# Kernel optimization log

Measured on AMD Instinct MI355X. Metric: run time of the kernel, lower is better.

The kernel has to match this reference:

```python
import jax, jax.numpy as jnp
import numpy as np

N = 50000
E = 800000
IN_C = 128
HID = 128
NUM_CLASSES = 64


def setup_inputs() -> dict:
    key = jax.random.key(0)
    ks = jax.random.split(key, 8)
    x = jax.random.normal(ks[0], (N, IN_C), dtype=jnp.float32)
    edge_index = jax.random.randint(ks[1], (2, E), 0, N, dtype=jnp.int64)
    # Xavier-uniform style weights stored as [in, out]; biases zero-init.
    def xavier(k, fan_in, fan_out):
        lim = float(np.sqrt(6.0 / (fan_in + fan_out)))
        return jax.random.uniform(k, (fan_in, fan_out), minval=-lim, maxval=lim, dtype=jnp.float32)
    W1 = xavier(ks[2], IN_C, HID)
    b1 = jnp.zeros((HID,), dtype=jnp.float32)
    W2 = xavier(ks[3], HID, HID)
    b2 = jnp.zeros((HID,), dtype=jnp.float32)
    W3 = xavier(ks[4], HID, NUM_CLASSES)
    b3 = jnp.zeros((NUM_CLASSES,), dtype=jnp.float32)
    return {"x": x, "edge_index": edge_index, "W1": W1, "b1": b1, "W2": W2, "b2": b2, "W3": W3, "b3": b3}


def _add_self_loops(edge_index, num_nodes):
    loops = jnp.arange(num_nodes, dtype=edge_index.dtype)
    row = jnp.concatenate([edge_index[0], loops])
    col = jnp.concatenate([edge_index[1], loops])
    return row, col


def _gcn_layer(x, row, col, dinv, W, b):
    # x: [N, Cin] -> h: [N, Cout]; symmetric-normalized scatter-add aggregation.
    h = x @ W
    norm = dinv[row] * dinv[col]              # [E']
    msg = norm[:, None] * h[row]              # gather + scale (dropout is a no-op in eval)
    out = jax.ops.segment_sum(msg, col, num_segments=x.shape[0])
    return out + b


def reference(x, edge_index, W1, b1, W2, b2, W3, b3):
    n = x.shape[0]
    row, col = _add_self_loops(edge_index, n)
    deg = jax.ops.segment_sum(jnp.ones_like(col, dtype=x.dtype), col, num_segments=n)
    dinv = jnp.where(deg > 0, deg ** -0.5, 0.0)
    h1 = jax.nn.relu(_gcn_layer(x, row, col, dinv, W1, b1))
    h2 = jax.nn.relu(_gcn_layer(h1, row, col, dinv, W2, b2))
    out = _gcn_layer(h2, row, col, dinv, W3, b3)
    return (h2, out)
```

## Files before the change

### kernel.cpp

```cpp
#include <hip/hip_runtime.h>
#include <hip/hip_bf16.h>


typedef float vf4 __attribute__((ext_vector_type(4)));
typedef unsigned vu4 __attribute__((ext_vector_type(4)));
typedef unsigned vu2 __attribute__((ext_vector_type(2)));
typedef short bf8v __attribute__((ext_vector_type(8)));
typedef float f4v __attribute__((ext_vector_type(4)));

constexpr int PCAP = 25000;
constexpr int NHB  = 64;

__device__ __forceinline__ float bits2f(unsigned u) {
    union { unsigned u; float f; } c; c.u = u; return c.f;
}
__device__ __forceinline__ unsigned short f2bfu(float v) {
    __hip_bfloat16 h = __float2bfloat16(v);
    union { __hip_bfloat16 h; unsigned short u; } c; c.h = h; return c.u;
}
__device__ __forceinline__ float bflo(unsigned d) { return bits2f(d << 16); }
__device__ __forceinline__ float bfhi(unsigned d) { return bits2f(d & 0xffff0000u); }

__global__ void detect_dtypes(const void* __restrict__ x,
                              const void* __restrict__ ei,
                              int* __restrict__ flags) {
    const int t = threadIdx.x;
    const int lane = t & 63;
    if (t < 64) {
        const unsigned short* p = (const unsigned short*)x;
        int e = (p[2 * (lane * 16)] >> 7) & 0xFF;
        unsigned long long m = __ballot(e < 100 || e > 140);
        if (lane == 0) flags[0] = (__popcll(m) > 16) ? 1 : 0;
    } else if (t < 128) {
        const int* p = (const int*)ei;
        unsigned long long m = __ballot(p[2 * (lane * 16) + 1] != 0);
        if (lane == 0) flags[1] = (__popcll(m) < 2) ? 1 : 0;
    }
}

__device__ __forceinline__ int edge_at(const void* ei, long long idx, bool i64) {
    return i64 ? (int)((const long long*)ei)[idx] : ((const int*)ei)[idx];
}

__global__ __launch_bounds__(1024) void hist_count(const void* __restrict__ ei,
                                                   int* __restrict__ row32,
                                                   int* __restrict__ col32,
                                                   unsigned* __restrict__ histg,
                                                   const int* __restrict__ flags,
                                                   int e, int epb, int pc) {
    __shared__ unsigned h[PCAP];
    const int t = threadIdx.x;
    const int b = blockIdx.x;
    for (int j = t; j < pc; j += 1024) h[j] = 0u;
    __syncthreads();
    const bool i64 = flags[1] != 0;
    const int base = b * epb;
    const int end = min(e, base + epb);
    for (int i = base + t; i < end; i += 1024) {
        int r = edge_at(ei, i, i64);
        int c = edge_at(ei, (long long)e + i, i64);
        row32[i] = r;
        col32[i] = c;
        atomicAdd(&h[c >> 1], (c & 1) ? 0x10000u : 1u);
    }
    __syncthreads();
    unsigned* out = histg + (size_t)b * pc;
    for (int j = t; j < pc; j += 1024) __builtin_nontemporal_store(h[j], &out[j]);
}

__global__ __launch_bounds__(256) void hist_scan(unsigned* __restrict__ histg,
                                                 int* __restrict__ cnt, int pc, int n) {
    __shared__ unsigned tile[NHB][65];
    const int t = threadIdx.x;
    const int c = t & 63;
    const int jc = blockIdx.x * 64 + c;
    for (int r = t >> 6; r < NHB; r += 4)
        tile[r][c] = (jc < pc) ? histg[(size_t)r * pc + jc] : 0u;
    __syncthreads();
    if (t < 64 && jc < pc) {
        unsigned run = 0;
        for (int r = 0; r < NHB; ++r) {
            unsigned v = tile[r][t];
            tile[r][t] = run;
            run += v;
        }
        int c0 = jc * 2;
        if (c0 < n) cnt[c0] = (int)(run & 0xffffu);
        if (c0 + 1 < n) cnt[c0 + 1] = (int)(run >> 16);
    }
    __syncthreads();
    for (int r = t >> 6; r < NHB; r += 4)
        if (jc < pc) __builtin_nontemporal_store(tile[r][c], &histg[(size_t)r * pc + jc]);
}

__global__ __launch_bounds__(1024) void scatter_fill(const int* __restrict__ row32,
                                                     const int* __restrict__ col32,
                                                     const unsigned* __restrict__ histg,
                                                     const int* __restrict__ off,
                                                     int* __restrict__ csr,
                                                     int e, int epb, int pc) {
    __shared__ unsigned h[PCAP];
    const int t = threadIdx.x;
    const int b = blockIdx.x;
    const unsigned* src = histg + (size_t)b * pc;
    for (int j = t; j < pc; j += 1024) h[j] = src[j];
    __syncthreads();
    const int base = b * epb;
    const int end = min(e, base + epb);
    for (int i = base + t; i < end; i += 1024) {
        int r = row32[i];
        int c = col32[i];
        unsigned old = atomicAdd(&h[c >> 1], (c & 1) ? 0x10000u : 1u);
        unsigned rank = (c & 1) ? (old >> 16) : (old & 0xffffu);
        csr[off[c] + (int)rank] = r;
    }
}

__global__ void convert_count(const void* __restrict__ ei,
                              int* __restrict__ row32, int* __restrict__ col32,
                              int* __restrict__ rank32,
                              int* __restrict__ cnt,
                              const int* __restrict__ flags, int e) {
    int i = blockIdx.x * 256 + threadIdx.x;
    if (i < e) {
        const bool i64 = flags[1] != 0;
        int r = edge_at(ei, i, i64);
        int c = edge_at(ei, (long long)e + i, i64);
        row32[i] = r;
        col32[i] = c;
        rank32[i] = atomicAdd(&cnt[c], 1);
    }
}

__global__ void fill_csr(const int* __restrict__ row32, const int* __restrict__ col32,
                         const int* __restrict__ rank32, const int* __restrict__ off,
                         int* __restrict__ csr_src, int e) {
    int i = blockIdx.x * 256 + threadIdx.x;
    if (i < e) {
        csr_src[off[col32[i]] + rank32[i]] = row32[i];
    }
}

__global__ __launch_bounds__(256) void deg_reduce(const int* __restrict__ cnt,
                                                  int* __restrict__ bsum, int n) {
    __shared__ int sm[4];
    const int t = threadIdx.x;
    int i = blockIdx.x * 256 + t;
    int v = (i < n) ? cnt[i] : 0;
#pragma unroll
    for (int d = 32; d >= 1; d >>= 1) v += __shfl_down(v, d);
    if ((t & 63) == 0) sm[t >> 6] = v;
    __syncthreads();
    if (t == 0) bsum[blockIdx.x] = sm[0] + sm[1] + sm[2] + sm[3];
}

__global__ __launch_bounds__(256) void scan_bsums(int* __restrict__ bsum, int nb) {
    __shared__ int sm[256];
    const int t = threadIdx.x;
    sm[t] = (t < nb) ? bsum[t] : 0;
    __syncthreads();
#pragma unroll
    for (int d = 1; d < 256; d <<= 1) {
        int v = (t >= d) ? sm[t - d] : 0;
        __syncthreads();
        sm[t] += v;
        __syncthreads();
    }
    if (t < nb) bsum[t] = (t == 0) ? 0 : sm[t - 1];
}

__global__ __launch_bounds__(256) void write_off(const int* __restrict__ cnt,
                                                 const int* __restrict__ bsum,
                                                 int* __restrict__ off,
                                                 float* __restrict__ dinv,
                                                 int n, int e_total) {
    __shared__ int sm[256];
    const int t = threadIdx.x;
    const int i = blockIdx.x * 256 + t;
    const int c = (i < n) ? cnt[i] : 0;
    sm[t] = c;
    __syncthreads();
#pragma unroll
    for (int d = 1; d < 256; d <<= 1) {
        int v = (t >= d) ? sm[t - d] : 0;
        __syncthreads();
        sm[t] += v;
        __syncthreads();
    }
    if (i < n) {
        int o = bsum[blockIdx.x] + sm[t] - c;
        off[i] = o;
        dinv[i] = rsqrtf((float)(c + 1));
        if (i == n - 1) off[n] = e_total;
    }
}

template <int COUT, bool XDYN>
__global__ __launch_bounds__(256) void gemm_mfma(const void* __restrict__ Xv,
                                                 const void* __restrict__ Wv,
                                                 const float* __restrict__ dinv,
                                                 unsigned short* __restrict__ G,
                                                 const int* __restrict__ flags, int n) {
    constexpr int WS = 132;
    __shared__ __align__(16) short Wt[COUT * WS];
    const int t = threadIdx.x;
    const bool f32 = flags[0] != 0;

    if (f32) {
        const float* W = (const float*)Wv;
        for (int i = t; i < 128 * COUT; i += 256) {
            int k = i / COUT, c = i % COUT;
            Wt[c * WS + k] = (short)f2bfu(W[i]);
        }
    } else {
        const short* W = (const short*)Wv;
        for (int i = t; i < 128 * COUT; i += 256) {
            int k = i / COUT, c = i % COUT;
            Wt[c * WS + k] = W[i];
        }
    }
    __syncthreads();

    const int w = t >> 6, l = t & 63;
    const int m = l & 15, q = l >> 4;
    const int row = blockIdx.x * 64 + w * 16 + m;
    const int xrow = min(row, n - 1);

    bf8v xf[4];
    if (XDYN && f32) {
        const float* X = (const float*)Xv;
#pragma unroll
        for (int ks = 0; ks < 4; ++ks) {
            const float4 a = *(const float4*)&X[(size_t)xrow * 128 + ks * 32 + q * 8];
            const float4 b = *(const float4*)&X[(size_t)xrow * 128 + ks * 32 + q * 8 + 4];
            bf8v v;
            v[0] = (short)f2bfu(a.x); v[1] = (short)f2bfu(a.y);
            v[2] = (short)f2bfu(a.z); v[3] = (short)f2bfu(a.w);
            v[4] = (short)f2bfu(b.x); v[5] = (short)f2bfu(b.y);
            v[6] = (short)f2bfu(b.z); v[7] = (short)f2bfu(b.w);
            xf[ks] = v;
        }
    } else {
        const short* X = (const short*)Xv;
#pragma unroll
        for (int ks = 0; ks < 4; ++ks)
            xf[ks] = *(const bf8v*)&X[(size_t)xrow * 128 + ks * 32 + q * 8];
    }
    const float dv = dinv[xrow];

#pragma unroll
    for (int ct = 0; ct < COUT / 16; ++ct) {
        f4v acc = {0.f, 0.f, 0.f, 0.f};
#pragma unroll
        for (int ks = 0; ks < 4; ++ks) {
            bf8v wf = *(const bf8v*)&Wt[(ct * 16 + m) * WS + ks * 32 + q * 8];
            acc = __builtin_amdgcn_mfma_f32_16x16x32_bf16(wf, xf[ks], acc, 0, 0, 0);
        }
        if (row < n) {
            vu2 u;
            u.x = (unsigned)f2bfu(dv * acc[0]) | ((unsigned)f2bfu(dv * acc[1]) << 16);
            u.y = (unsigned)f2bfu(dv * acc[2]) | ((unsigned)f2bfu(dv * acc[3]) << 16);
            *(vu2*)&G[(size_t)row * COUT + ct * 16 + q * 4] = u;
        }
    }
}

template <int CPL, bool RELU, bool WWS, bool WOUT>
__global__ __launch_bounds__(256) void aggregate(const unsigned* __restrict__ Gd,
                                                 const int* __restrict__ off,
                                                 const int* __restrict__ csr_src,
                                                 const float* __restrict__ dinv,
                                                 const void* __restrict__ bias,
                                                 unsigned* __restrict__ Hws,
                                                 void* __restrict__ outp,
                                                 long long out_off,
                                                 const int* __restrict__ flags, int n) {
    const int gw = (int)((blockIdx.x * 256u + threadIdx.x) >> 6);
    const int lane = threadIdx.x & 63;
    if (gw >= n) return;
    constexpr int C = CPL * 64;
    constexpr int LPG = (CPL == 2) ? 16 : 8;
    constexpr int GROUPS = 64 / LPG;
    constexpr int RD = C / 2;
    const int g = lane / LPG;
    const int li = lane % LPG;
    const int e0 = off[gw];
    const int e1 = off[gw + 1];
    const float d = dinv[gw];

    float acc[8];
    {
        uint4 sv = *(const uint4*)&Gd[(size_t)gw * RD + li * 4];
        const float ms = (g == 0) ? 1.f : 0.f;
        acc[0] = ms * bflo(sv.x); acc[1] = ms * bfhi(sv.x);
        acc[2] = ms * bflo(sv.y); acc[3] = ms * bfhi(sv.y);
        acc[4] = ms * bflo(sv.z); acc[5] = ms * bfhi(sv.z);
        acc[6] = ms * bflo(sv.w); acc[7] = ms * bfhi(sv.w);
    }

    for (int bs = e0; bs < e1; bs += 64) {
        const int cnt = min(64, e1 - bs);
        const int myidx = (bs + lane < e1) ? csr_src[bs + lane] : 0;
        for (int j = 0; j < cnt; j += 2 * GROUPS) {
#pragma unroll
            for (int u = 0; u < 2; ++u) {
                const int eb = j + u * GROUPS + g;
                const int jj = min(eb, cnt - 1);
                const int s = __shfl(myidx, jj);
                const float m = (eb < cnt) ? 1.f : 0.f;
                uint4 v = *(const uint4*)&Gd[(size_t)s * RD + li * 4];
                acc[0] = fmaf(m, bflo(v.x), acc[0]);
                acc[1] = fmaf(m, bfhi(v.x), acc[1]);
                acc[2] = fmaf(m, bflo(v.y), acc[2]);
                acc[3] = fmaf(m, bfhi(v.y), acc[3]);
                acc[4] = fmaf(m, bflo(v.z), acc[4]);
                acc[5] = fmaf(m, bfhi(v.z), acc[5]);
                acc[6] = fmaf(m, bflo(v.w), acc[6]);
                acc[7] = fmaf(m, bfhi(v.w), acc[7]);
            }
        }
    }

#pragma unroll
    for (int mask = LPG; mask <= 32; mask <<= 1)
#pragma unroll
        for (int i = 0; i < 8; ++i) acc[i] += __shfl_xor(acc[i], mask);

    const bool f32 = flags[0] != 0;
    float bvf[8];
    if (f32) {
        const float* B = (const float*)bias;
        const float4 b0 = *(const float4*)&B[li * 8];
        const float4 b1 = *(const float4*)&B[li * 8 + 4];
        bvf[0] = b0.x; bvf[1] = b0.y; bvf[2] = b0.z; bvf[3] = b0.w;
        bvf[4] = b1.x; bvf[5] = b1.y; bvf[6] = b1.z; bvf[7] = b1.w;
    } else {
        const uint4 bv = *(const uint4*)&((const unsigned*)bias)[li * 4];
        bvf[0] = bflo(bv.x); bvf[1] = bfhi(bv.x);
        bvf[2] = bflo(bv.y); bvf[3] = bfhi(bv.y);
        bvf[4] = bflo(bv.z); bvf[5] = bfhi(bv.z);
        bvf[6] = bflo(bv.w); bvf[7] = bfhi(bv.w);
    }
    float o[8];
#pragma unroll
    for (int i = 0; i < 8; ++i) {
        o[i] = d * acc[i] + bvf[i];
        if (RELU) o[i] = fmaxf(o[i], 0.f);
    }

    if (g == 0) {
        if constexpr (WWS) {
            vu4 u;
            u.x = (unsigned)f2bfu(o[0]) | ((unsigned)f2bfu(o[1]) << 16);
            u.y = (unsigned)f2bfu(o[2]) | ((unsigned)f2bfu(o[3]) << 16);
            u.z = (unsigned)f2bfu(o[4]) | ((unsigned)f2bfu(o[5]) << 16);
            u.w = (unsigned)f2bfu(o[6]) | ((unsigned)f2bfu(o[7]) << 16);
            unsigned* hb = Hws + (size_t)gw * RD + li * 4;
            __builtin_nontemporal_store(u, (vu4*)hb);
        }
        if constexpr (WOUT) {
            if (f32) {
                float* po = (float*)outp + out_off + (size_t)gw * C + li * 8;
                vf4 w0 = {o[0], o[1], o[2], o[3]};
                vf4 w1 = {o[4], o[5], o[6], o[7]};
                __builtin_nontemporal_store(w0, (vf4*)po);
                __builtin_nontemporal_store(w1, (vf4*)po + 1);
            } else {
                vu4 u;
                u.x = (unsigned)f2bfu(o[0]) | ((unsigned)f2bfu(o[1]) << 16);
                u.y = (unsigned)f2bfu(o[2]) | ((unsigned)f2bfu(o[3]) << 16);
                u.z = (unsigned)f2bfu(o[4]) | ((unsigned)f2bfu(o[5]) << 16);
                u.w = (unsigned)f2bfu(o[6]) | ((unsigned)f2bfu(o[7]) << 16);
                unsigned* ob = (unsigned*)outp + (out_off >> 1) + (size_t)gw * RD + li * 4;
                __builtin_nontemporal_store(u, (vu4*)ob);
            }
        }
    }
}

extern "C" void kernel_launch(void* const* d_in, const int* in_sizes, int n_in,
                              void* d_out, int out_size, void* d_ws, size_t ws_size,
                              hipStream_t stream) {
    const void* x  = d_in[0];
    const void* ei = d_in[1];
    const void* W1 = d_in[2];
    const void* b1 = d_in[3];
    const void* W2 = d_in[4];
    const void* b2 = d_in[5];
    const void* W3 = d_in[6];
    const void* b3 = d_in[7];

    const int N = in_sizes[0] / 128;
    const int E = in_sizes[1] / 2;

    char* p = (char*)d_ws;
    auto take = [&](size_t bytes) {
        char* q = p;
        p += (bytes + 255) & ~(size_t)255;
        return q;
    };
    const int pc  = (N + 1) / 2;
    const int epb = (E + NHB - 1) / NHB;
    const bool histpath = (pc <= PCAP) && (epb < 65536);

    int*      flags = (int*)take(64);
    int*      cnt   = (int*)take((size_t)N * 4);
    int*      bsum  = (int*)take(1024);
    int*      off   = (int*)take((size_t)(N + 1) * 4);
    float*    dinv  = (float*)take((size_t)N * 4);
    int*      row32 = (int*)take((size_t)E * 4);
    int*      col32 = (int*)take((size_t)E * 4);
    int*      csr   = (int*)take((size_t)E * 4);
    unsigned* histg = (unsigned*)take(histpath ? (size_t)NHB * pc * 4 : 0);
    int*      rank32 = (int*)take(histpath ? 0 : (size_t)E * 4);
    unsigned short* bufA = (unsigned short*)take((size_t)N * 128 * 2);
    unsigned short* bufB = (unsigned short*)take((size_t)N * 128 * 2);
    (void)n_in; (void)out_size; (void)ws_size;

    const int nb = (N + 255) / 256;
    const int eb = (E + 255) / 256;

    detect_dtypes<<<1, 128, 0, stream>>>(x, ei, flags);

    if (histpath) {
        hist_count<<<NHB, 1024, 0, stream>>>(ei, row32, col32, histg, flags, E, epb, pc);
        hist_scan<<<(pc + 63) / 64, 256, 0, stream>>>(histg, cnt, pc, N);
        deg_reduce<<<nb, 256, 0, stream>>>(cnt, bsum, N);
        scan_bsums<<<1, 256, 0, stream>>>(bsum, nb);
        write_off<<<nb, 256, 0, stream>>>(cnt, bsum, off, dinv, N, E);
        scatter_fill<<<NHB, 1024, 0, stream>>>(row32, col32, histg, off, csr, E, epb, pc);
    } else {
        hipMemsetAsync(cnt, 0, (size_t)N * 4, stream);
        convert_count<<<eb, 256, 0, stream>>>(ei, row32, col32, rank32, cnt, flags, E);
        deg_reduce<<<nb, 256, 0, stream>>>(cnt, bsum, N);
        scan_bsums<<<1, 256, 0, stream>>>(bsum, nb);
        write_off<<<nb, 256, 0, stream>>>(cnt, bsum, off, dinv, N, E);
        fill_csr<<<eb, 256, 0, stream>>>(row32, col32, rank32, off, csr, E);
    }

    const int gb = (N + 63) / 64;
    const int ab = (N + 3) / 4;

    gemm_mfma<128, true><<<gb, 256, 0, stream>>>(x, W1, dinv, bufA, flags, N);
    aggregate<2, true, true, false><<<ab, 256, 0, stream>>>((const unsigned*)bufA, off, csr, dinv, b1, (unsigned*)bufB, nullptr, 0, flags, N);
    gemm_mfma<128, false><<<gb, 256, 0, stream>>>(bufB, W2, dinv, bufA, flags, N);
    aggregate<2, true, true, true><<<ab, 256, 0, stream>>>((const unsigned*)bufA, off, csr, dinv, b2, (unsigned*)bufB, d_out, 0, flags, N);
    gemm_mfma<64, false><<<gb, 256, 0, stream>>>(bufB, W3, dinv, bufA, flags, N);
    aggregate<1, false, false, true><<<ab, 256, 0, stream>>>((const unsigned*)bufA, off, csr, dinv, b3, nullptr, d_out, (long long)N * 128, flags, N);
}
```

Baseline: 277.1 us.

## Fuse degree reduce into hist scan, drop row32/col32 staging, double hist blocks

The CSR build no longer stages int32 row/col copies. hist_count reads only the column array, and scatter_fill re-reads the original edge_index directly. hist_scan now processes 128 packed columns (256 nodes) per block and emits per-block degree sums, which removes the separate deg_reduce launch. The number of histogram blocks doubles to 128 for more parallelism, at the cost of a larger histogram buffer and a longer serial scan per column. Re-reading the int64 edge indices in scatter_fill may cost more bandwidth than reading the int32 copies did.

```diff
diff --git a/kernel.cpp b/kernel.cpp
--- a/kernel.cpp
+++ b/kernel.cpp
@@ -9,7 +9,8 @@
 typedef float f4v __attribute__((ext_vector_type(4)));
 
 constexpr int PCAP = 25000;
-constexpr int NHB  = 64;
+constexpr int NHB  = 128;
+constexpr int SCB  = 128;
 
 __device__ __forceinline__ float bits2f(unsigned u) {
     union { unsigned u; float f; } c; c.u = u; return c.f;
@@ -43,8 +44,6 @@
 }
 
 __global__ __launch_bounds__(1024) void hist_count(const void* __restrict__ ei,
-                                                   int* __restrict__ row32,
-                                                   int* __restrict__ col32,
                                                    unsigned* __restrict__ histg,
                                                    const int* __restrict__ flags,
                                                    int e, int epb, int pc) {
@@ -52,6 +51,72 @@
     const int t = threadIdx.x;
     const int b = blockIdx.x;
     for (int j = t; j < pc; j += 1024) h[j] = 0u;
+    __syncthreads();
+    const bool i64 = flags[1] != 0;
+    const int base = b * epb;
+    const int end = min(e, base + epb);
+    for (int i = base + t; i < end; i += 1024) {
+        int c = edge_at(ei, (long long)e + i, i64);
+        atomicAdd(&h[c >> 1], (c & 1) ? 0x10000u : 1u);
+    }
+    __syncthreads();
+    unsigned* out = histg + (size_t)b * pc;
+    for (int j = t; j < pc; j += 1024) __builtin_nontemporal_store(h[j], &out[j]);
+}
+
+__global__ __launch_bounds__(256) void hist_scan(unsigned* __restrict__ histg,
+                                                 int* __restrict__ cnt,
+                                                 int* __restrict__ bsum,
+                                                 int pc, int n) {
+    __shared__ unsigned tile[NHB][SCB + 1];
+    __shared__ int red[2];
+    const int t = threadIdx.x;
+    const int b = blockIdx.x;
+    const int jc0 = b * SCB;
+    for (int idx = t; idx < NHB * SCB; idx += 256) {
+        int r = idx >> 7;
+        int c = idx & (SCB - 1);
+        int jc = jc0 + c;
+        tile[r][c] = (jc < pc) ? histg[(size_t)r * pc + jc] : 0u;
+    }
+    __syncthreads();
+    int deg = 0;
+    if (t < SCB) {
+        unsigned run = 0;
+        for (int r = 0; r < NHB; ++r) {
+            unsigned v = tile[r][t];
+            tile[r][t] = run;
+            run += v;
+        }
+        int c0 = (jc0 + t) * 2;
+        if (c0 < n) cnt[c0] = (int)(run & 0xffffu);
+        if (c0 + 1 < n) cnt[c0 + 1] = (int)(run >> 16);
+        deg = (int)(run & 0xffffu) + (int)(run >> 16);
+    }
+#pragma unroll
+    for (int d2 = 32; d2 >= 1; d2 >>= 1) deg += __shfl_down(deg, d2);
+    if ((t & 63) == 0 && t < SCB) red[t >> 6] = deg;
+    __syncthreads();
+    if (t == 0) bsum[b] = red[0] + red[1];
+    for (int idx = t; idx < NHB * SCB; idx += 256) {
+        int r = idx >> 7;
+        int c = idx & (SCB - 1);
+        int jc = jc0 + c;
+        if (jc < pc) __builtin_nontemporal_store(tile[r][c], &histg[(size_t)r * pc + jc]);
+    }
+}
+
+__global__ __launch_bounds__(1024) void scatter_fill(const void* __restrict__ ei,
+                                                     const unsigned* __restrict__ histg,
+                                                     const int* __restrict__ off,
+                                                     int* __restrict__ csr,
+                                                     const int* __restrict__ flags,
+                                                     int e, int epb, int pc) {
+    __shared__ unsigned h[PCAP];
+    const int t = threadIdx.x;
+    const int b = blockIdx.x;
+    const unsigned* src = histg + (size_t)b * pc;
+    for (int j = t; j < pc; j += 1024) h[j] = src[j];
     __syncthreads();
     const bool i64 = flags[1] != 0;
     const int base = b * epb;
@@ -59,57 +124,6 @@
     for (int i = base + t; i < end; i += 1024) {
         int r = edge_at(ei, i, i64);
         int c = edge_at(ei, (long long)e + i, i64);
-        row32[i] = r;
-        col32[i] = c;
-        atomicAdd(&h[c >> 1], (c & 1) ? 0x10000u : 1u);
-    }
-    __syncthreads();
-    unsigned* out = histg + (size_t)b * pc;
-    for (int j = t; j < pc; j += 1024) __builtin_nontemporal_store(h[j], &out[j]);
-}
-
-__global__ __launch_bounds__(256) void hist_scan(unsigned* __restrict__ histg,
-                                                 int* __restrict__ cnt, int pc, int n) {
-    __shared__ unsigned tile[NHB][65];
-    const int t = threadIdx.x;
-    const int c = t & 63;
-    const int jc = blockIdx.x * 64 + c;
-    for (int r = t >> 6; r < NHB; r += 4)
-        tile[r][c] = (jc < pc) ? histg[(size_t)r * pc + jc] : 0u;
-    __syncthreads();
-    if (t < 64 && jc < pc) {
-        unsigned run = 0;
-        for (int r = 0; r < NHB; ++r) {
-            unsigned v = tile[r][t];
-            tile[r][t] = run;
-            run += v;
-        }
-        int c0 = jc * 2;
-        if (c0 < n) cnt[c0] = (int)(run & 0xffffu);
-        if (c0 + 1 < n) cnt[c0 + 1] = (int)(run >> 16);
-    }
-    __syncthreads();
-    for (int r = t >> 6; r < NHB; r += 4)
-        if (jc < pc) __builtin_nontemporal_store(tile[r][c], &histg[(size_t)r * pc + jc]);
-}
-
-__global__ __launch_bounds__(1024) void scatter_fill(const int* __restrict__ row32,
-                                                     const int* __restrict__ col32,
-                                                     const unsigned* __restrict__ histg,
-                                                     const int* __restrict__ off,
-                                                     int* __restrict__ csr,
-                                                     int e, int epb, int pc) {
-    __shared__ unsigned h[PCAP];
-    const int t = threadIdx.x;
-    const int b = blockIdx.x;
-    const unsigned* src = histg + (size_t)b * pc;
-    for (int j = t; j < pc; j += 1024) h[j] = src[j];
-    __syncthreads();
-    const int base = b * epb;
-    const int end = min(e, base + epb);
-    for (int i = base + t; i < end; i += 1024) {
-        int r = row32[i];
-        int c = col32[i];
         unsigned old = atomicAdd(&h[c >> 1], (c & 1) ? 0x10000u : 1u);
         unsigned rank = (c & 1) ? (old >> 16) : (old & 0xffffu);
         csr[off[c] + (int)rank] = r;
@@ -408,10 +422,10 @@
     int*      bsum  = (int*)take(1024);
     int*      off   = (int*)take((size_t)(N + 1) * 4);
     float*    dinv  = (float*)take((size_t)N * 4);
-    int*      row32 = (int*)take((size_t)E * 4);
-    int*      col32 = (int*)take((size_t)E * 4);
     int*      csr   = (int*)take((size_t)E * 4);
     unsigned* histg = (unsigned*)take(histpath ? (size_t)NHB * pc * 4 : 0);
+    int*      row32 = (int*)take(histpath ? 0 : (size_t)E * 4);
+    int*      col32 = (int*)take(histpath ? 0 : (size_t)E * 4);
     int*      rank32 = (int*)take(histpath ? 0 : (size_t)E * 4);
     unsigned short* bufA = (unsigned short*)take((size_t)N * 128 * 2);
     unsigned short* bufB = (unsigned short*)take((size_t)N * 128 * 2);
@@ -423,12 +437,11 @@
     detect_dtypes<<<1, 128, 0, stream>>>(x, ei, flags);
 
     if (histpath) {
-        hist_count<<<NHB, 1024, 0, stream>>>(ei, row32, col32, histg, flags, E, epb, pc);
-        hist_scan<<<(pc + 63) / 64, 256, 0, stream>>>(histg, cnt, pc, N);
-        deg_reduce<<<nb, 256, 0, stream>>>(cnt, bsum, N);
+        hist_count<<<NHB, 1024, 0, stream>>>(ei, histg, flags, E, epb, pc);
+        hist_scan<<<nb, 256, 0, stream>>>(histg, cnt, bsum, pc, N);
         scan_bsums<<<1, 256, 0, stream>>>(bsum, nb);
         write_off<<<nb, 256, 0, stream>>>(cnt, bsum, off, dinv, N, E);
-        scatter_fill<<<NHB, 1024, 0, stream>>>(row32, col32, histg, off, csr, E, epb, pc);
+        scatter_fill<<<NHB, 1024, 0, stream>>>(ei, histg, off, csr, flags, E, epb, pc);
     } else {
         hipMemsetAsync(cnt, 0, (size_t)N * 4, stream);
         convert_count<<<eb, 256, 0, stream>>>(ei, row32, col32, rank32, cnt, flags, E);
```

Result: no change. 277.6 us (+0.2%).

## Raise histogram block count to 256 and parallelize per-column scan across threads

Applied to the files above, without the earlier changes.

The number of histogram blocks NHB grows from 64 to 256, so hist_count and scatter_fill each run on 256 blocks instead of 64. To cope with the taller histogram, hist_scan now handles 32 columns per block and splits each column's 256 rows into 8 segments, one warp each. It does a segment-sum pass, a small scan over the segment sums, and then a local exclusive scan per segment, instead of one thread serially scanning every row. The per-block histogram buffer gets 4x larger, which adds global traffic in exchange for more CU parallelism in counting and filling.

```diff
diff --git a/kernel.cpp b/kernel.cpp
--- a/kernel.cpp
+++ b/kernel.cpp
@@ -8,8 +8,9 @@
 typedef short bf8v __attribute__((ext_vector_type(8)));
 typedef float f4v __attribute__((ext_vector_type(4)));
 
-constexpr int PCAP = 25000;
-constexpr int NHB  = 64;
+constexpr int PCAP  = 25000;
+constexpr int NHB   = 256;
+constexpr int SCOLS = 32;
 
 __device__ __forceinline__ float bits2f(unsigned u) {
     union { unsigned u; float f; } c; c.u = u; return c.f;
@@ -70,27 +71,52 @@
 
 __global__ __launch_bounds__(256) void hist_scan(unsigned* __restrict__ histg,
                                                  int* __restrict__ cnt, int pc, int n) {
-    __shared__ unsigned tile[NHB][65];
-    const int t = threadIdx.x;
-    const int c = t & 63;
-    const int jc = blockIdx.x * 64 + c;
-    for (int r = t >> 6; r < NHB; r += 4)
+    __shared__ unsigned tile[NHB][SCOLS + 1];
+    __shared__ unsigned segsum[8][SCOLS + 1];
+    const int t = threadIdx.x;
+    const int jc0 = blockIdx.x * SCOLS;
+    for (int idx = t; idx < NHB * SCOLS; idx += 256) {
+        int r = idx >> 5, c = idx & 31;
+        int jc = jc0 + c;
         tile[r][c] = (jc < pc) ? histg[(size_t)r * pc + jc] : 0u;
-    __syncthreads();
-    if (t < 64 && jc < pc) {
+    }
+    __syncthreads();
+    const int c = t & 31, s = t >> 5;
+    {
         unsigned run = 0;
-        for (int r = 0; r < NHB; ++r) {
-            unsigned v = tile[r][t];
-            tile[r][t] = run;
+#pragma unroll
+        for (int k = 0; k < 32; ++k) run += tile[s * 32 + k][c];
+        segsum[s][c] = run;
+    }
+    __syncthreads();
+    if (t < 32) {
+        unsigned run = 0;
+#pragma unroll
+        for (int sg = 0; sg < 8; ++sg) {
+            unsigned v = segsum[sg][t];
+            segsum[sg][t] = run;
             run += v;
         }
-        int c0 = jc * 2;
+        int c0 = (jc0 + t) * 2;
         if (c0 < n) cnt[c0] = (int)(run & 0xffffu);
         if (c0 + 1 < n) cnt[c0 + 1] = (int)(run >> 16);
     }
     __syncthreads();
-    for (int r = t >> 6; r < NHB; r += 4)
-        if (jc < pc) __builtin_nontemporal_store(tile[r][c], &histg[(size_t)r * pc + jc]);
+    {
+        unsigned run = segsum[s][c];
+#pragma unroll
+        for (int k = 0; k < 32; ++k) {
+            unsigned v = tile[s * 32 + k][c];
+            tile[s * 32 + k][c] = run;
+            run += v;
+        }
+    }
+    __syncthreads();
+    for (int idx = t; idx < NHB * SCOLS; idx += 256) {
+        int r = idx >> 5, c2 = idx & 31;
+        int jc = jc0 + c2;
+        if (jc < pc) __builtin_nontemporal_store(tile[r][c2], &histg[(size_t)r * pc + jc]);
+    }
 }
 
 __global__ __launch_bounds__(1024) void scatter_fill(const int* __restrict__ row32,
@@ -424,7 +450,7 @@
 
     if (histpath) {
         hist_count<<<NHB, 1024, 0, stream>>>(ei, row32, col32, histg, flags, E, epb, pc);
-        hist_scan<<<(pc + 63) / 64, 256, 0, stream>>>(histg, cnt, pc, N);
+        hist_scan<<<(pc + SCOLS - 1) / SCOLS, 256, 0, stream>>>(histg, cnt, pc, N);
         deg_reduce<<<nb, 256, 0, stream>>>(cnt, bsum, N);
         scan_bsums<<<1, 256, 0, stream>>>(bsum, nb);
         write_off<<<nb, 256, 0, stream>>>(cnt, bsum, off, dinv, N, E);
```

After: 268.2 us. 1.03x faster.
